# Kernel optimization log

Measured on AMD Instinct MI355X. Metric: run time of the kernel, lower is better.

The kernel has to match this reference:

```python
import jax, jax.numpy as jnp
import numpy as np

B, T, D = 32, 512, 64   # batch, timesteps, latent dim
H, S = 64, 4096         # hidden_size, state_dim
EPS = 1e-6              # flax LayerNorm default epsilon


def _glorot(k, shape):
    lim = np.sqrt(6.0 / (shape[0] + shape[1])).astype(np.float32)
    return jax.random.uniform(k, shape, jnp.float32, -lim, lim)


def setup_inputs() -> dict:
    key = jax.random.key(0)
    ks = jax.random.split(key, 7)
    # gate order in the fused 4H axis: i, f, g, o ; flax inits f-gate bias to 1
    bh = jnp.concatenate([jnp.zeros((H,)), jnp.ones((H,)), jnp.zeros((2 * H,))]).astype(jnp.float32)
    return {
        "enc_outputs": jax.random.normal(ks[0], (B, T, D), jnp.float32),
        "Wx": _glorot(ks[1], (D, 4 * H)),   # input->gates, no bias (flax dense_i)
        "Wh": _glorot(ks[2], (H, 4 * H)),   # hidden->gates
        "bh": bh,
        "W1": _glorot(ks[3], (H, 2 * H)), "b1": jnp.zeros((2 * H,), jnp.float32),
        "g1": jnp.ones((2 * H,), jnp.float32), "be1": jnp.zeros((2 * H,), jnp.float32),
        "W2": _glorot(ks[4], (2 * H, 2 * H)), "b2": jnp.zeros((2 * H,), jnp.float32),
        "g2": jnp.ones((2 * H,), jnp.float32), "be2": jnp.zeros((2 * H,), jnp.float32),
        "Wo": _glorot(ks[5], (2 * H, S)), "bo": jnp.zeros((S,), jnp.float32),
    }


def _layernorm(x, g, b):
    m = x.mean(-1, keepdims=True)
    v = ((x - m) ** 2).mean(-1, keepdims=True)
    return (x - m) * jax.lax.rsqrt(v + EPS) * g + b


def _lstm(enc, Wx, Wh, bh):
    # precompute all input projections in one big GEMM: [B,T,4H]
    xg = jnp.einsum('btd,dg->btg', enc, Wx)

    def step(carry, x_t):
        c, h = carry
        z = x_t + h @ Wh + bh              # [B,4H]
        i, f, g, o = jnp.split(z, 4, axis=-1)
        c = jax.nn.sigmoid(f) * c + jax.nn.sigmoid(i) * jnp.tanh(g)
        h = jax.nn.sigmoid(o) * jnp.tanh(c)
        return (c, h), h

    b = enc.shape[0]
    init = (jnp.zeros((b, H), enc.dtype), jnp.zeros((b, H), enc.dtype))
    _, hs = jax.lax.scan(step, init, xg.swapaxes(0, 1))  # hs: [T,B,H]
    return hs.swapaxes(0, 1)                              # [B,T,H]


def reference(enc_outputs, Wx, Wh, bh, W1, b1, g1, be1, W2, b2, g2, be2, Wo, bo):
    b, t, _ = enc_outputs.shape
    dec = _lstm(enc_outputs, Wx, Wh, bh)            # [B,T,H]
    flat = dec.reshape(b * t, H)
    h = jax.nn.gelu(_layernorm(flat @ W1 + b1, g1, be1))   # flax gelu: tanh approx
    # dropout deterministic (train=False) -> identity
    h = jax.nn.gelu(_layernorm(h @ W2 + b2, g2, be2))
    out = h @ Wo + bo                                # [B*T,S]
    return out.reshape(b, t, S)
```

## Files before the change

kernel.cpp:

```cpp
#include <hip/hip_runtime.h>
#include <hip/hip_bf16.h>

#define T_ 512

typedef __attribute__((ext_vector_type(8))) short short8;
typedef __attribute__((ext_vector_type(4))) float f32x4;

__device__ __forceinline__ float fast_rcp(float x){ return __builtin_amdgcn_rcpf(x); }
__device__ __forceinline__ float sigmoid_f(float x){
  return fast_rcp(1.f + __expf(-x));
}
__device__ __forceinline__ float tanh_f(float x){
  return fmaf(2.f, fast_rcp(1.f + __expf(-2.f*x)), -1.f);
}
__device__ __forceinline__ float gelu_f(float x){
  float u = 0.7978845608028654f*(x + 0.044715f*x*x*x);
  return 0.5f*x*(1.f + tanh_f(u));
}

__global__ __launch_bounds__(256) void k_xg(const float* __restrict__ enc,
                                            const float* __restrict__ Wx,
                                            const float* __restrict__ bh,
                                            float* __restrict__ xg)
{
  __shared__ __align__(16) float es[64*64];
  int j = threadIdx.x;
  int g = blockIdx.x;
  const float* encg = enc + (size_t)g*64*64;
  for (int idx = j; idx < 64*64; idx += 256) es[idx] = encg[idx];
  float wx[64];
#pragma unroll
  for (int k = 0; k < 64; ++k) wx[k] = Wx[k*256 + j];
  float bj = bh[j];
  __syncthreads();
  float* xo = xg + (size_t)g*64*256;
  for (int r = 0; r < 64; ++r){
    const float4* e4 = (const float4*)(es + r*64);
    float z0 = bj, z1 = 0.f, z2 = 0.f, z3 = 0.f;
#pragma unroll
    for (int k4 = 0; k4 < 16; ++k4){
      float4 v = e4[k4];
      z0 = fmaf(v.x, wx[4*k4+0], z0);
      z1 = fmaf(v.y, wx[4*k4+1], z1);
      z2 = fmaf(v.z, wx[4*k4+2], z2);
      z3 = fmaf(v.w, wx[4*k4+3], z3);
    }
    xo[r*256 + j] = (z0+z1)+(z2+z3);
  }
}

__global__ __launch_bounds__(256) void k_lstm(const float* __restrict__ xg,
                                              const float* __restrict__ Wh,
                                              float* __restrict__ hs)
{
  __shared__ __align__(16) float hb[2][64];
  int tid = threadIdx.x;
  int w = tid >> 6, l = tid & 63;
  int m = w*16 + (l & 15);
  int g = l >> 4;
  int j = g*64 + m;
  int b = blockIdx.x;
  float wh[64];
#pragma unroll
  for (int k = 0; k < 64; ++k) wh[k] = Wh[k*256 + j];
  bool upd = (l < 16);
  float c = 0.f;
  if (tid < 64) hb[0][tid] = 0.f;
  const float* xr = xg + (size_t)b*T_*256;
  float* ho = hs + (size_t)b*T_*64;
  float xn0 = xr[j];
  float xn1 = xr[256 + j];
  float xn2 = xr[512 + j];
  float xn3 = xr[768 + j];
  __syncthreads();

#define LSTM_STEP(tt, xn)                                                     \
  {                                                                           \
    const float4* h4 = (const float4*)hb[(tt) & 1];                           \
    float z0 = (xn), z1 = 0.f, z2 = 0.f, z3 = 0.f;                            \
    if ((tt) + 4 < T_) (xn) = xr[(size_t)((tt) + 4)*256 + j];                 \
    _Pragma("unroll")                                                         \
    for (int k4 = 0; k4 < 16; ++k4){                                          \
      float4 v = h4[k4];                                                      \
      z0 = fmaf(v.x, wh[4*k4+0], z0);                                         \
      z1 = fmaf(v.y, wh[4*k4+1], z1);                                         \
      z2 = fmaf(v.z, wh[4*k4+2], z2);                                         \
      z3 = fmaf(v.w, wh[4*k4+3], z3);                                         \
    }                                                                         \
    float z = (z0+z1)+(z2+z3);                                                \
    float zB = __shfl_xor(z, 16);                        \
    float zC = __shfl_xor(z, 32);                        \
    float zD = __shfl_xor(z, 48);                        \
    if (upd){                                                                 \
      c = sigmoid_f(zB)*c + sigmoid_f(z)*tanh_f(zC);                          \
      float h = sigmoid_f(zD)*tanh_f(c);                                      \
      hb[((tt)+1) & 1][m] = h;                                                \
      ho[(size_t)(tt)*64 + m] = h;                                            \
    }                                                                         \
    __syncthreads();                                                          \
  }

  for (int t = 0; t < T_; t += 4){
    LSTM_STEP(t,   xn0);
    LSTM_STEP(t+1, xn1);
    LSTM_STEP(t+2, xn2);
    LSTM_STEP(t+3, xn3);
  }
#undef LSTM_STEP
}

__global__ __launch_bounds__(256) void k_mlp(const float* __restrict__ hs,
    const float* __restrict__ W1, const float* __restrict__ b1,
    const float* __restrict__ g1, const float* __restrict__ be1,
    const float* __restrict__ W2, const float* __restrict__ b2,
    const float* __restrict__ g2, const float* __restrict__ be2,
    __hip_bfloat16* __restrict__ h2g)
{
  __shared__ __align__(16) float xs[2][64];
  __shared__ __align__(16) float vs[2][128];
  __shared__ float red[2][2][2];
  int tid = threadIdx.x;
  int jj = tid & 127, rg = tid >> 7;
  int lane = tid & 63;
  int whalf = (tid >> 6) & 1;
  float w1c[64], w2c[128];
#pragma unroll
  for (int k = 0; k < 64; ++k) w1c[k] = W1[k*128 + jj];
#pragma unroll
  for (int k = 0; k < 128; ++k) w2c[k] = W2[k*128 + jj];
  float b1j = b1[jj], g1j = g1[jj], be1j = be1[jj];
  float b2j = b2[jj], g2j = g2[jj], be2j = be2[jj];
  int base = blockIdx.x * 64;
  for (int p = 0; p < 32; ++p){
    int r = base + p*2 + rg;
    if (whalf == 0) xs[rg][lane] = hs[(size_t)r*64 + lane];
    __syncthreads();
    float a0 = b1j, a1 = 0.f;
    const float4* x4 = (const float4*)xs[rg];
#pragma unroll
    for (int k4 = 0; k4 < 16; ++k4){
      float4 v = x4[k4];
      a0 = fmaf(v.x, w1c[4*k4+0], a0);
      a1 = fmaf(v.y, w1c[4*k4+1], a1);
      a0 = fmaf(v.z, w1c[4*k4+2], a0);
      a1 = fmaf(v.w, w1c[4*k4+3], a1);
    }
    float a = a0 + a1;
    float s1 = a, s2 = a*a;
#pragma unroll
    for (int off = 32; off > 0; off >>= 1){
      s1 += __shfl_xor(s1, off, 64);
      s2 += __shfl_xor(s2, off, 64);
    }
    if (lane == 0){ red[rg][whalf][0] = s1; red[rg][whalf][1] = s2; }
    __syncthreads();
    s1 = red[rg][0][0] + red[rg][1][0];
    s2 = red[rg][0][1] + red[rg][1][1];
    float mean = s1*(1.f/128.f);
    float var  = s2*(1.f/128.f) - mean*mean;
    float rstd = rsqrtf(var + 1e-6f);
    float y = gelu_f((a - mean)*rstd*g1j + be1j);
    vs[rg][jj] = y;
    __syncthreads();
    float c0 = b2j, c1 = 0.f;
    const float4* v4 = (const float4*)vs[rg];
#pragma unroll
    for (int k4 = 0; k4 < 32; ++k4){
      float4 v = v4[k4];
      c0 = fmaf(v.x, w2c[4*k4+0], c0);
      c1 = fmaf(v.y, w2c[4*k4+1], c1);
      c0 = fmaf(v.z, w2c[4*k4+2], c0);
      c1 = fmaf(v.w, w2c[4*k4+3], c1);
    }
    float cc = c0 + c1;
    float t1 = cc, t2 = cc*cc;
#pragma unroll
    for (int off = 32; off > 0; off >>= 1){
      t1 += __shfl_xor(t1, off, 64);
      t2 += __shfl_xor(t2, off, 64);
    }
    if (lane == 0){ red[rg][whalf][0] = t1; red[rg][whalf][1] = t2; }
    __syncthreads();
    t1 = red[rg][0][0] + red[rg][1][0];
    t2 = red[rg][0][1] + red[rg][1][1];
    mean = t1*(1.f/128.f);
    var  = t2*(1.f/128.f) - mean*mean;
    rstd = rsqrtf(var + 1e-6f);
    float z = gelu_f((cc - mean)*rstd*g2j + be2j);
    h2g[(size_t)r*128 + jj] = __float2bfloat16(z);
  }
}

__global__ __launch_bounds__(256) void k_wot(const float* __restrict__ Wo,
                                             __hip_bfloat16* __restrict__ WoT)
{
  __shared__ __hip_bfloat16 tl[64][130];
  int tid = threadIdx.x;
  int n0 = blockIdx.x * 64;
  for (int idx = tid; idx < 64*128; idx += 256){
    int k = idx >> 6, nl = idx & 63;
    tl[nl][k] = __float2bfloat16(Wo[(size_t)k*4096 + n0 + nl]);
  }
  __syncthreads();
  for (int idx = tid; idx < 64*128; idx += 256){
    int nl = idx >> 7, k = idx & 127;
    WoT[(size_t)(n0 + nl)*128 + k] = tl[nl][k];
  }
}

__global__ __launch_bounds__(256) void k_out(const __hip_bfloat16* __restrict__ h2g,
                                             const __hip_bfloat16* __restrict__ WoT,
                                             const float* __restrict__ bo,
                                             float* __restrict__ out)
{
  int bid = blockIdx.x;
  int Mb = bid >> 5, Nb = bid & 31;
  int tid = threadIdx.x;
  int w = tid >> 6, l = tid & 63;
  int wm = w >> 1, wn = w & 1;
  int m0 = Mb*128 + wm*64, n0 = Nb*128 + wn*64;
  int lr = l & 15, lk = (l >> 4)*8;
  f32x4 acc[4][4] = {};
  const short* A  = (const short*)WoT;
  const short* Bp = (const short*)h2g;
#pragma unroll
  for (int kk = 0; kk < 4; ++kk){
    int ko = kk*32 + lk;
    short8 av[4], bv[4];
#pragma unroll
    for (int i = 0; i < 4; ++i) av[i] = *(const short8*)(A  + (size_t)(n0 + i*16 + lr)*128 + ko);
#pragma unroll
    for (int i = 0; i < 4; ++i) bv[i] = *(const short8*)(Bp + (size_t)(m0 + i*16 + lr)*128 + ko);
#pragma unroll
    for (int fm = 0; fm < 4; ++fm)
#pragma unroll
      for (int fn = 0; fn < 4; ++fn)
        acc[fm][fn] = __builtin_amdgcn_mfma_f32_16x16x32_bf16(av[fn], bv[fm], acc[fm][fn], 0, 0, 0);
  }
  int nb_ = (l >> 4)*4;
#pragma unroll
  for (int fn = 0; fn < 4; ++fn){
    f32x4 bia = *(const f32x4*)(bo + n0 + fn*16 + nb_);
#pragma unroll
    for (int fm = 0; fm < 4; ++fm){
      size_t row = (size_t)(m0 + fm*16 + lr)*4096;
      __builtin_nontemporal_store(acc[fm][fn] + bia, (f32x4*)(out + row + n0 + fn*16 + nb_));
    }
  }
}

extern "C" void kernel_launch(void* const* d_in, const int* in_sizes, int n_in,
                              void* d_out, int out_size, void* d_ws, size_t ws_size,
                              hipStream_t stream)
{
  const float* enc = (const float*)d_in[0];
  const float* Wx  = (const float*)d_in[1];
  const float* Wh  = (const float*)d_in[2];
  const float* bh  = (const float*)d_in[3];
  const float* W1  = (const float*)d_in[4];
  const float* b1  = (const float*)d_in[5];
  const float* g1  = (const float*)d_in[6];
  const float* be1 = (const float*)d_in[7];
  const float* W2  = (const float*)d_in[8];
  const float* b2  = (const float*)d_in[9];
  const float* g2  = (const float*)d_in[10];
  const float* be2 = (const float*)d_in[11];
  const float* Wo  = (const float*)d_in[12];
  const float* bo  = (const float*)d_in[13];
  float* out = (float*)d_out;

  const size_t xg_bytes = (size_t)16384*256*4;
  const size_t hs_bytes = (size_t)16384*64*4;
  const size_t h2_bytes = (size_t)16384*128*2;
  const size_t wt_bytes = (size_t)4096*128*2;
  char* ws = (char*)d_ws;
  float *xg, *hs; __hip_bfloat16 *h2g, *WoT;
  if (ws_size >= xg_bytes + hs_bytes + h2_bytes + wt_bytes){
    xg  = (float*)ws;
    hs  = (float*)(ws + xg_bytes);
    h2g = (__hip_bfloat16*)(ws + xg_bytes + hs_bytes);
    WoT = (__hip_bfloat16*)(ws + xg_bytes + hs_bytes + h2_bytes);
  } else {
    xg  = (float*)d_out;
    hs  = (float*)((char*)d_out + xg_bytes);
    h2g = (__hip_bfloat16*)ws;
    WoT = (__hip_bfloat16*)(ws + h2_bytes);
  }

  k_xg  <<<256,  256, 0, stream>>>(enc, Wx, bh, xg);
  k_wot <<<64,   256, 0, stream>>>(Wo, WoT);
  k_lstm<<<32,   256, 0, stream>>>(xg, Wh, hs);
  k_mlp <<<256,  256, 0, stream>>>(hs, W1, b1, g1, be1, W2, b2, g2, be2, h2g);
  k_out <<<4096, 256, 0, stream>>>(h2g, WoT, bo, out);
}
```

Before: 471.4 us.

## Broadcast LSTM hidden state via readlane and exchange gate preactivations through LDS

Restructures the LSTM recurrence. Each wave now computes the gate nonlinearities for all 64 hidden units redundantly, taking the four gate preactivations from shared memory. It then broadcasts h inside the wave with readlane to form the next step's preactivations, instead of reading h from LDS and shuffling gates. The aim is to cut LDS traffic and cross-lane shuffles on the serial critical path while keeping one barrier per step. In exchange each wave repeats the transcendental work, and the 64 readlanes produce scalar operands. Launch bounds also gain a min-blocks hint of 1 on every kernel, which may change register allocation.

```diff
diff --git a/kernel.cpp b/kernel.cpp
--- a/kernel.cpp
+++ b/kernel.cpp
@@ -17,11 +17,14 @@
   float u = 0.7978845608028654f*(x + 0.044715f*x*x*x);
   return 0.5f*x*(1.f + tanh_f(u));
 }
-
-__global__ __launch_bounds__(256) void k_xg(const float* __restrict__ enc,
-                                            const float* __restrict__ Wx,
-                                            const float* __restrict__ bh,
-                                            float* __restrict__ xg)
+__device__ __forceinline__ float readlane_f(float v, int lane){
+  return __int_as_float(__builtin_amdgcn_readlane(__float_as_int(v), lane));
+}
+
+__global__ __launch_bounds__(256, 1) void k_xg(const float* __restrict__ enc,
+                                               const float* __restrict__ Wx,
+                                               const float* __restrict__ bh,
+                                               float* __restrict__ xg)
 {
   __shared__ __align__(16) float es[64*64];
   int j = threadIdx.x;
@@ -49,53 +52,46 @@
   }
 }
 
-__global__ __launch_bounds__(256) void k_lstm(const float* __restrict__ xg,
-                                              const float* __restrict__ Wh,
-                                              float* __restrict__ hs)
-{
-  __shared__ __align__(16) float hb[2][64];
+__global__ __launch_bounds__(256, 1) void k_lstm(const float* __restrict__ xg,
+                                                 const float* __restrict__ Wh,
+                                                 float* __restrict__ hs)
+{
+  __shared__ __align__(16) float zsm[2][256];
   int tid = threadIdx.x;
   int w = tid >> 6, l = tid & 63;
-  int m = w*16 + (l & 15);
-  int g = l >> 4;
-  int j = g*64 + m;
+  int j = tid;
   int b = blockIdx.x;
   float wh[64];
 #pragma unroll
   for (int k = 0; k < 64; ++k) wh[k] = Wh[k*256 + j];
-  bool upd = (l < 16);
   float c = 0.f;
-  if (tid < 64) hb[0][tid] = 0.f;
   const float* xr = xg + (size_t)b*T_*256;
   float* ho = hs + (size_t)b*T_*64;
-  float xn0 = xr[j];
-  float xn1 = xr[256 + j];
-  float xn2 = xr[512 + j];
-  float xn3 = xr[768 + j];
+  float xn0 = xr[1*256 + j];
+  float xn1 = xr[2*256 + j];
+  float xn2 = xr[3*256 + j];
+  float xn3 = xr[4*256 + j];
+  zsm[0][j] = xr[j];
   __syncthreads();
 
 #define LSTM_STEP(tt, xn)                                                     \
   {                                                                           \
-    const float4* h4 = (const float4*)hb[(tt) & 1];                           \
-    float z0 = (xn), z1 = 0.f, z2 = 0.f, z3 = 0.f;                            \
-    if ((tt) + 4 < T_) (xn) = xr[(size_t)((tt) + 4)*256 + j];                 \
-    _Pragma("unroll")                                                         \
-    for (int k4 = 0; k4 < 16; ++k4){                                          \
-      float4 v = h4[k4];                                                      \
-      z0 = fmaf(v.x, wh[4*k4+0], z0);                                         \
-      z1 = fmaf(v.y, wh[4*k4+1], z1);                                         \
-      z2 = fmaf(v.z, wh[4*k4+2], z2);                                         \
-      z3 = fmaf(v.w, wh[4*k4+3], z3);                                         \
-    }                                                                         \
-    float z = (z0+z1)+(z2+z3);                                                \
-    float zB = __shfl_xor(z, 16);                        \
-    float zC = __shfl_xor(z, 32);                        \
-    float zD = __shfl_xor(z, 48);                        \
-    if (upd){                                                                 \
-      c = sigmoid_f(zB)*c + sigmoid_f(z)*tanh_f(zC);                          \
-      float h = sigmoid_f(zD)*tanh_f(c);                                      \
-      hb[((tt)+1) & 1][m] = h;                                                \
-      ho[(size_t)(tt)*64 + m] = h;                                            \
+    const float* zb = zsm[(tt) & 1];                                          \
+    float zi = zb[l], zf = zb[64+l], zg_ = zb[128+l], zo = zb[192+l];         \
+    c = sigmoid_f(zf)*c + sigmoid_f(zi)*tanh_f(zg_);                          \
+    float h = sigmoid_f(zo)*tanh_f(c);                                        \
+    if (w == 0) ho[(size_t)(tt)*64 + l] = h;                                  \
+    if ((tt) + 1 < T_){                                                       \
+      float z0 = (xn), z1 = 0.f, z2 = 0.f, z3 = 0.f;                          \
+      if ((tt) + 5 < T_) (xn) = xr[(size_t)((tt)+5)*256 + j];                 \
+      _Pragma("unroll")                                                       \
+      for (int k = 0; k < 64; k += 4){                                        \
+        z0 = fmaf(readlane_f(h, k+0), wh[k+0], z0);                           \
+        z1 = fmaf(readlane_f(h, k+1), wh[k+1], z1);                           \
+        z2 = fmaf(readlane_f(h, k+2), wh[k+2], z2);                           \
+        z3 = fmaf(readlane_f(h, k+3), wh[k+3], z3);                           \
+      }                                                                       \
+      zsm[((tt)+1) & 1][j] = (z0+z1)+(z2+z3);                                 \
     }                                                                         \
     __syncthreads();                                                          \
   }
@@ -109,7 +105,7 @@
 #undef LSTM_STEP
 }
 
-__global__ __launch_bounds__(256) void k_mlp(const float* __restrict__ hs,
+__global__ __launch_bounds__(256, 1) void k_mlp(const float* __restrict__ hs,
     const float* __restrict__ W1, const float* __restrict__ b1,
     const float* __restrict__ g1, const float* __restrict__ be1,
     const float* __restrict__ W2, const float* __restrict__ b2,
@@ -191,8 +187,8 @@
   }
 }
 
-__global__ __launch_bounds__(256) void k_wot(const float* __restrict__ Wo,
-                                             __hip_bfloat16* __restrict__ WoT)
+__global__ __launch_bounds__(256, 1) void k_wot(const float* __restrict__ Wo,
+                                                __hip_bfloat16* __restrict__ WoT)
 {
   __shared__ __hip_bfloat16 tl[64][130];
   int tid = threadIdx.x;
@@ -208,10 +204,10 @@
   }
 }
 
-__global__ __launch_bounds__(256) void k_out(const __hip_bfloat16* __restrict__ h2g,
-                                             const __hip_bfloat16* __restrict__ WoT,
-                                             const float* __restrict__ bo,
-                                             float* __restrict__ out)
+__global__ __launch_bounds__(256, 1) void k_out(const __hip_bfloat16* __restrict__ h2g,
+                                                const __hip_bfloat16* __restrict__ WoT,
+                                                const float* __restrict__ bo,
+                                                float* __restrict__ out)
 {
   int bid = blockIdx.x;
   int Mb = bid >> 5, Nb = bid & 31;
```

Measured after the change: 426.0 us. 1.11x faster.
